# Optimization experiments

Hardware: AMD Instinct MI355X
Metric: run time of the kernel (lower is better)

Reference implementation:

```python
import jax, jax.numpy as jnp
import numpy as np

B, N, C, H, K, R = 128, 512, 7, 64, 16, 2
EPS = 1e-5


def setup_inputs() -> dict:
    key = jax.random.key(0)
    ks = jax.random.split(key, 8)
    def w(k, shape, scale):
        return jax.random.normal(k, shape, jnp.float32) * scale
    return {
        'x':    jax.random.normal(ks[0], (B, C, N), jnp.float32),
        # track_mlp: Conv1d(C->H, bias=False) + BN + ReLU, Conv1d(H->H) + BN + ReLU
        'w_t1': w(ks[1], (H, C), 0.3),
        'g_t1': jnp.ones((H,), jnp.float32), 'b_t1': jnp.zeros((H,), jnp.float32),
        'w_t2': w(ks[2], (H, H), 0.15),
        'g_t2': jnp.ones((H,), jnp.float32), 'b_t2': jnp.zeros((H,), jnp.float32),
        # per-round neighbor MLP: Conv1d(2H->H, bias=False) + BN + ReLU (stacked over rounds)
        'w_nb': w(ks[3], (R, H, 2 * H), 0.1),
        'g_nb': jnp.ones((R, H), jnp.float32), 'b_nb': jnp.zeros((R, H), jnp.float32),
        # scorer: Conv1d(H->H, bias=False) + BN + ReLU, Conv1d(H->1, bias=True)
        'w_s1': w(ks[4], (H, H), 0.15),
        'g_s1': jnp.ones((H,), jnp.float32), 'b_s1': jnp.zeros((H,), jnp.float32),
        'w_s2': w(ks[5], (1, H), 0.15), 'b_s2': jnp.zeros((1,), jnp.float32),
    }


def _conv1x1(w, h):
    # Conv1d with kernel_size=1, no bias: (O,C) x (B,C,N) -> (B,O,N)
    return jnp.einsum('oc,bcn->bon', w, h)


def _bn(h, g, b):
    # eval-mode BatchNorm1d with running_mean=0, running_var=1
    s = g / jnp.sqrt(1.0 + EPS)
    return h * s[None, :, None] + b[None, :, None]


def _knn_idx(h, k):
    # h: (B,H,N); squared euclidean distances in feature space, k nearest (incl. self)
    sq = jnp.sum(h * h, axis=1)                       # (B,N)
    inner = jnp.einsum('bhn,bhm->bnm', h, h)          # (B,N,N)
    d = sq[:, :, None] + sq[:, None, :] - 2.0 * inner  # (B,N,N)
    _, idx = jax.lax.top_k(-d, k)                     # (B,N,K)
    return jax.lax.stop_gradient(idx)


def _edgeconv_round(h, w, g, b, k):
    idx = _knn_idx(h, k)                              # (B,N,K)
    # gather neighbor features: (B,H,1,N) indexed along last axis -> (B,H,N,K)
    nbr = jnp.take_along_axis(h[:, :, None, :], idx[:, None, :, :], axis=3)
    hc = h[:, :, :, None]                             # (B,H,N,1)
    edge = jnp.concatenate([jnp.broadcast_to(hc, nbr.shape), nbr - hc], axis=1)  # (B,2H,N,K)
    bsz, twoh, n, kk = edge.shape
    m = _conv1x1(w, edge.reshape(bsz, twoh, n * kk))  # (B,H,N*K)
    m = jax.nn.relu(_bn(m, g, b)).reshape(bsz, -1, n, kk)
    return jnp.max(m, axis=3)                          # (B,H,N) max aggregation


def reference(x, w_t1, g_t1, b_t1, w_t2, g_t2, b_t2, w_nb, g_nb, b_nb,
              w_s1, g_s1, b_s1, w_s2, b_s2):
    # shared per-track MLP
    h = jax.nn.relu(_bn(_conv1x1(w_t1, x), g_t1, b_t1))
    h = jax.nn.relu(_bn(_conv1x1(w_t2, h), g_t2, b_t2))
    # kNN message-passing rounds (EdgeConv with max aggregation)
    for r in range(w_nb.shape[0]):
        h = _edgeconv_round(h, w_nb[r], g_nb[r], b_nb[r], K)
    # scorer head -> per-track logits (B,1,N)
    h = jax.nn.relu(_bn(_conv1x1(w_s1, h), g_s1, b_s1))
    logits = _conv1x1(w_s2, h) + b_s2[None, :, None]
    return logits
```

## Files before the change

### kernel.cpp

```cpp
#include <hip/hip_runtime.h>
#include <math.h>

#define Bn 128
#define Nn 512
#define Cc 7
#define Hh 64
#define Kk 16
#define Rr 2
#define EPSf 1e-5f

typedef __attribute__((ext_vector_type(8))) short bf16x8;
typedef __attribute__((ext_vector_type(4))) float f32x4;

#define PLN ((size_t)4194304)

__device__ __forceinline__ void split3(float a, short &hs, short &ms, short &ls) {
    unsigned u  = __float_as_uint(a);
    unsigned hu = u & 0xFFFF0000u;
    float r1 = a - __uint_as_float(hu);
    unsigned mu = __float_as_uint(r1) & 0xFFFF0000u;
    float r2 = r1 - __uint_as_float(mu);
    unsigned lu = __float_as_uint(r2) & 0xFFFF0000u;
    hs = (short)(hu >> 16); ms = (short)(mu >> 16); ls = (short)(lu >> 16);
}

#define MFMA6(acc, AH, AM, AL, BH, BM, BL) \
    acc = __builtin_amdgcn_mfma_f32_16x16x32_bf16(AL, BH, acc, 0, 0, 0); \
    acc = __builtin_amdgcn_mfma_f32_16x16x32_bf16(AM, BM, acc, 0, 0, 0); \
    acc = __builtin_amdgcn_mfma_f32_16x16x32_bf16(AH, BL, acc, 0, 0, 0); \
    acc = __builtin_amdgcn_mfma_f32_16x16x32_bf16(AM, BH, acc, 0, 0, 0); \
    acc = __builtin_amdgcn_mfma_f32_16x16x32_bf16(AH, BM, acc, 0, 0, 0); \
    acc = __builtin_amdgcn_mfma_f32_16x16x32_bf16(AH, BH, acc, 0, 0, 0);

__global__ void k_prep(const float* __restrict__ w_nb, const float* __restrict__ w_t2,
                       const float* __restrict__ w_s1, short* __restrict__ wS)
{
    int i = blockIdx.x * 256 + threadIdx.x;
    short h_, m_, l_;
    if (i < 8192) {
        int r = i >> 12, oc = i & 4095;
        int o = oc >> 6, c = oc & 63;
        const float* wr = w_nb + (size_t)r * Hh * 2 * Hh + (size_t)o * 2 * Hh;
        float wc = wr[c], wd = wr[Hh + c];
        short* base = wS + (size_t)r * 6 * 4096;
        split3(wd, h_, m_, l_);
        base[0 * 4096 + oc] = h_; base[1 * 4096 + oc] = m_; base[2 * 4096 + oc] = l_;
        split3(wc - wd, h_, m_, l_);
        base[3 * 4096 + oc] = h_; base[4 * 4096 + oc] = m_; base[5 * 4096 + oc] = l_;
    } else {
        int which = (i - 8192) >> 12;
        int oc = i & 4095;
        const float* src = which ? w_s1 : w_t2;
        short* base = wS + (size_t)(12 + which * 3) * 4096;
        split3(src[oc], h_, m_, l_);
        base[0 * 4096 + oc] = h_; base[1 * 4096 + oc] = m_; base[2 * 4096 + oc] = l_;
    }
}

__global__ __launch_bounds__(256) void k_t12(
    const float* __restrict__ x,
    const float* __restrict__ w1, const float* __restrict__ g1, const float* __restrict__ b1,
    const short* __restrict__ wS2, const float* __restrict__ g2, const float* __restrict__ b2,
    short* __restrict__ hS, float* __restrict__ sq)
{
    __shared__ short wLDS[3][64 * 80];
    __shared__ short h1S[3][16 * 80];
    __shared__ float sqP[16][4];

    int t  = threadIdx.x;
    int p0 = blockIdx.x * 16;
    int b  = p0 >> 9, n0 = p0 & 511;

#pragma unroll
    for (int it = 0; it < 6; ++it) {
        int f = it * 256 + t;
        int plane = f >> 9, i8 = f & 511;
        int o = i8 >> 3, c8 = i8 & 7;
        uint4 v = ((const uint4*)(wS2 + (size_t)plane * 4096))[i8];
        *(uint4*)&wLDS[plane][o * 80 + c8 * 8] = v;
    }

    {
        int pt = t & 15, ow = t >> 4;
        const float inv = rsqrtf(1.0f + EPSf);
        float xv[Cc];
#pragma unroll
        for (int c = 0; c < Cc; ++c)
            xv[c] = x[(b * Cc + c) * Nn + n0 + pt];
#pragma unroll
        for (int j = 0; j < 4; ++j) {
            int o = ow + 16 * j;
            float acc = 0.0f;
#pragma unroll
            for (int c = 0; c < Cc; ++c)
                acc = fmaf(w1[o * Cc + c], xv[c], acc);
            acc = fmaf(acc, g1[o] * inv, b1[o]);
            acc = fmaxf(acc, 0.0f);
            short hs_, ms_, ls_;
            split3(acc, hs_, ms_, ls_);
            h1S[0][pt * 80 + o] = hs_;
            h1S[1][pt * 80 + o] = ms_;
            h1S[2][pt * 80 + o] = ls_;
        }
    }
    __syncthreads();

    int wv = t >> 6, lane = t & 63, col = lane & 15, quad = lane >> 4;
    const float inv = rsqrtf(1.0f + EPSf);

    f32x4 acc = (f32x4){0.f, 0.f, 0.f, 0.f};
#pragma unroll
    for (int ks = 0; ks < 2; ++ks) {
        int aoff = ks * 32 + quad * 8;
        bf16x8 AH = *(bf16x8*)&h1S[0][col * 80 + aoff];
        bf16x8 AM = *(bf16x8*)&h1S[1][col * 80 + aoff];
        bf16x8 AL = *(bf16x8*)&h1S[2][col * 80 + aoff];
        int boff = (wv * 16 + col) * 80 + aoff;
        bf16x8 BH = *(bf16x8*)&wLDS[0][boff];
        bf16x8 BM = *(bf16x8*)&wLDS[1][boff];
        bf16x8 BL = *(bf16x8*)&wLDS[2][boff];
        MFMA6(acc, AH, AM, AL, BH, BM, BL)
    }

    int o = wv * 16 + col;
    float sc = g2[o] * inv, bo = b2[o];
    float s4[4];
#pragma unroll
    for (int r = 0; r < 4; ++r) {
        int pt = quad * 4 + r;
        float a2 = fmaf(acc[r], sc, bo);
        a2 = fmaxf(a2, 0.0f);
        short hs_, ms_, ls_;
        split3(a2, hs_, ms_, ls_);
        size_t rowp = (size_t)(p0 + pt) * Hh + o;
        hS[0 * PLN + rowp] = hs_;
        hS[1 * PLN + rowp] = ms_;
        hS[2 * PLN + rowp] = ls_;
        s4[r] = a2 * a2;
    }
#pragma unroll
    for (int sh = 1; sh < 16; sh <<= 1) {
#pragma unroll
        for (int r = 0; r < 4; ++r) s4[r] += __shfl_xor(s4[r], sh, 64);
    }
    if (col == 0) {
#pragma unroll
        for (int r = 0; r < 4; ++r) sqP[quad * 4 + r][wv] = s4[r];
    }
    __syncthreads();
    if (t < 16) sq[p0 + t] = sqP[t][0] + sqP[t][1] + sqP[t][2] + sqP[t][3];
}

__global__ __launch_bounds__(256, 4) void k_knn(
    const short* __restrict__ hS, const float* __restrict__ sq, int* __restrict__ idxout)
{
    int xcd = blockIdx.x & 7;
    int s_  = blockIdx.x >> 3;
    int b   = xcd + ((s_ >> 5) << 3);
    int n0  = (s_ & 31) << 4;
    int t   = threadIdx.x;

    __shared__ unsigned int keysLDS[16 * 512];
    __shared__ float sqS[512];

    if (t < 128) ((float4*)sqS)[t] = ((const float4*)(sq + (size_t)b * Nn))[t];
    __syncthreads();

    int wv = t >> 6, lane = t & 63, col = lane & 15, quad = lane >> 4;
    const size_t rowbase = (size_t)b * Nn * Hh;

    bf16x8 AH[2], AM[2], AL[2];
    {
        const short* crow = hS + rowbase + (size_t)(n0 + col) * Hh;
#pragma unroll
        for (int ks = 0; ks < 2; ++ks) {
            int aoff = ks * 32 + quad * 8;
            AH[ks] = *(const bf16x8*)(crow + 0 * PLN + aoff);
            AM[ks] = *(const bf16x8*)(crow + 1 * PLN + aoff);
            AL[ks] = *(const bf16x8*)(crow + 2 * PLN + aoff);
        }
    }
    float sqcr[4];
#pragma unroll
    for (int r_ = 0; r_ < 4; ++r_) sqcr[r_] = sqS[n0 + quad * 4 + r_];

    for (int i = 0; i < 8; ++i) {
        int nt = wv * 8 + i;
        const short* prow = hS + rowbase + (size_t)(nt * 16 + col) * Hh;
        f32x4 acc = (f32x4){0.f, 0.f, 0.f, 0.f};
#pragma unroll
        for (int ks = 0; ks < 2; ++ks) {
            int aoff = ks * 32 + quad * 8;
            bf16x8 BH = *(const bf16x8*)(prow + 0 * PLN + aoff);
            bf16x8 BM = *(const bf16x8*)(prow + 1 * PLN + aoff);
            bf16x8 BL = *(const bf16x8*)(prow + 2 * PLN + aoff);
            MFMA6(acc, AH[ks], AM[ks], AL[ks], BH, BM, BL)
        }
        float sqp = sqS[nt * 16 + col];
#pragma unroll
        for (int r_ = 0; r_ < 4; ++r_) {
            int ctr = quad * 4 + r_;
            float d = sqcr[r_] + sqp - 2.0f * acc[r_];
            unsigned int u = __float_as_uint(d);
            u = ((int)u < 0) ? ~u : (u | 0x80000000u);
            keysLDS[ctr * 512 + nt * 16 + col] = u;
        }
    }
    __syncthreads();

    unsigned int kk[4][8];
    int rr[4][8];
#pragma unroll
    for (int s = 0; s < 4; ++s) {
        int jj = wv * 4 + s;
        const uint4* kp = (const uint4*)&keysLDS[jj * 512 + (lane << 3)];
        uint4 A = kp[0], Bq = kp[1];
        kk[s][0] = A.x;  kk[s][1] = A.y;  kk[s][2] = A.z;  kk[s][3] = A.w;
        kk[s][4] = Bq.x; kk[s][5] = Bq.y; kk[s][6] = Bq.z; kk[s][7] = Bq.w;
#pragma unroll
        for (int q = 0; q < 8; ++q) rr[s][q] = q;
    }

#define CE(s, i, j_) { \
    bool sw = (kk[s][i] > kk[s][j_]) || (kk[s][i] == kk[s][j_] && rr[s][i] > rr[s][j_]); \
    unsigned int tk = sw ? kk[s][i] : kk[s][j_]; kk[s][i] = sw ? kk[s][j_] : kk[s][i]; kk[s][j_] = tk; \
    int tr = sw ? rr[s][i] : rr[s][j_]; rr[s][i] = sw ? rr[s][j_] : rr[s][i]; rr[s][j_] = tr; }
#pragma unroll
    for (int s = 0; s < 4; ++s) {
        CE(s,0,1) CE(s,2,3) CE(s,4,5) CE(s,6,7)
        CE(s,0,2) CE(s,1,3) CE(s,4,6) CE(s,5,7)
        CE(s,1,2) CE(s,5,6)
        CE(s,0,4) CE(s,1,5) CE(s,2,6) CE(s,3,7)
        CE(s,2,4) CE(s,3,5)
        CE(s,1,2) CE(s,3,4) CE(s,5,6)
    }
#undef CE

    int outbase[4];
#pragma unroll
    for (int s = 0; s < 4; ++s) outbase[s] = (b * Nn + n0 + wv * 4 + s) * Kk;

    for (int iter = 0; iter < Kk; ++iter) {
        unsigned int mv[4];
#pragma unroll
        for (int s = 0; s < 4; ++s) mv[s] = kk[s][0];
#define DSTEP(ctrl) { \
        _Pragma("unroll") \
        for (int s = 0; s < 4; ++s) { \
            unsigned int ov = (unsigned int)__builtin_amdgcn_update_dpp((int)mv[s], (int)mv[s], ctrl, 0xF, 0xF, false); \
            mv[s] = (ov < mv[s]) ? ov : mv[s]; } }
        DSTEP(0xB1)
        DSTEP(0x4E)
        DSTEP(0x124)
        DSTEP(0x128)
        DSTEP(0x142)
        DSTEP(0x143)
#undef DSTEP
        unsigned int m[4];
#pragma unroll
        for (int s = 0; s < 4; ++s)
            m[s] = (unsigned int)__builtin_amdgcn_readlane((int)mv[s], 63);
#pragma unroll
        for (int s = 0; s < 4; ++s) {
            unsigned long long bal = __ballot(kk[s][0] == m[s]);
            int wn = __ffsll(bal) - 1;
            if (lane == wn) {
                idxout[outbase[s] + iter] = (lane << 3) + rr[s][0];
#pragma unroll
                for (int q = 0; q < 7; ++q) { kk[s][q] = kk[s][q + 1]; rr[s][q] = rr[s][q + 1]; }
                kk[s][7] = 0xFFFFFFFFu;
            }
        }
    }
}

__global__ __launch_bounds__(256, 4) void k_edge(
    const short* __restrict__ hS,
    const int* __restrict__ idx,
    const short* __restrict__ wS,
    const float* __restrict__ g, const float* __restrict__ bb_,
    short* __restrict__ hSout, float* __restrict__ sqout)
{
    __shared__ short wLDS[3][64 * 72];
    __shared__ float baseS[16 * 68];
    __shared__ int   idxS[256];

    int t   = threadIdx.x;
    int xcd = blockIdx.x & 7;
    int s_  = blockIdx.x >> 3;
    int b   = xcd + ((s_ >> 5) << 3);
    int p0  = b * Nn + ((s_ & 31) << 4);

    idxS[t] = idx[p0 * Kk + t];
#pragma unroll
    for (int it = 0; it < 6; ++it) {
        int f = it * 256 + t;
        int plane = f >> 9;
        int i8 = f & 511;
        int o = i8 >> 3, c8 = i8 & 7;
        uint4 v = ((const uint4*)(wS + (size_t)(3 + plane) * 4096))[i8];
        *(uint4*)&wLDS[plane][o * 72 + c8 * 8] = v;
    }
    __syncthreads();

    int wv = t >> 6, lane = t & 63, col = lane & 15, quad = lane >> 4;

    {
        f32x4 bacc = (f32x4){0.f, 0.f, 0.f, 0.f};
        const short* hrow = hS + (size_t)(p0 + col) * Hh;
#pragma unroll
        for (int ks = 0; ks < 2; ++ks) {
            int aoff = ks * 32 + quad * 8;
            bf16x8 AH = *(const bf16x8*)(hrow + 0 * PLN + aoff);
            bf16x8 AM = *(const bf16x8*)(hrow + 1 * PLN + aoff);
            bf16x8 AL = *(const bf16x8*)(hrow + 2 * PLN + aoff);
            int boff = (wv * 16 + col) * 72 + aoff;
            bf16x8 BH = *(bf16x8*)&wLDS[0][boff];
            bf16x8 BM = *(bf16x8*)&wLDS[1][boff];
            bf16x8 BL = *(bf16x8*)&wLDS[2][boff];
            MFMA6(bacc, AH, AM, AL, BH, BM, BL)
        }
#pragma unroll
        for (int r_ = 0; r_ < 4; ++r_)
            baseS[(quad * 4 + r_) * 68 + wv * 16 + col] = bacc[r_];
    }
    __syncthreads();

#pragma unroll
    for (int it = 0; it < 6; ++it) {
        int f = it * 256 + t;
        int plane = f >> 9;
        int i8 = f & 511;
        int o = i8 >> 3, c8 = i8 & 7;
        uint4 v = ((const uint4*)(wS + (size_t)plane * 4096))[i8];
        *(uint4*)&wLDS[plane][o * 72 + c8 * 8] = v;
    }
    __syncthreads();

    const float inv = rsqrtf(1.0f + EPSf);
    float scv[4], bov[4];
#pragma unroll
    for (int nt = 0; nt < 4; ++nt) {
        scv[nt] = g[nt * 16 + col] * inv;
        bov[nt] = bb_[nt * 16 + col];
    }

    for (int pr = 0; pr < 2; ++pr) {
        bf16x8 A[2][2][3];
#pragma unroll
        for (int pt2 = 0; pt2 < 2; ++pt2) {
            int pl = wv * 4 + pr * 2 + pt2;
            int j = idxS[pl * 16 + col];
            const short* nrow = hS + ((size_t)(b * Nn) + j) * Hh;
#pragma unroll
            for (int ks = 0; ks < 2; ++ks) {
                int aoff = ks * 32 + quad * 8;
                A[pt2][ks][0] = *(const bf16x8*)(nrow + 0 * PLN + aoff);
                A[pt2][ks][1] = *(const bf16x8*)(nrow + 1 * PLN + aoff);
                A[pt2][ks][2] = *(const bf16x8*)(nrow + 2 * PLN + aoff);
            }
        }

        f32x4 acc[2][4];
#pragma unroll
        for (int pt2 = 0; pt2 < 2; ++pt2)
#pragma unroll
            for (int nt = 0; nt < 4; ++nt)
                acc[pt2][nt] = (f32x4){0.f, 0.f, 0.f, 0.f};

#pragma unroll
        for (int ks = 0; ks < 2; ++ks)
#pragma unroll
            for (int nt = 0; nt < 4; ++nt) {
                int boff = (nt * 16 + col) * 72 + ks * 32 + quad * 8;
                bf16x8 BH = *(bf16x8*)&wLDS[0][boff];
                bf16x8 BM = *(bf16x8*)&wLDS[1][boff];
                bf16x8 BL = *(bf16x8*)&wLDS[2][boff];
#pragma unroll
                for (int pt2 = 0; pt2 < 2; ++pt2) {
                    f32x4 a = acc[pt2][nt];
                    MFMA6(a, A[pt2][ks][0], A[pt2][ks][1], A[pt2][ks][2], BH, BM, BL)
                    acc[pt2][nt] = a;
                }
            }

#pragma unroll
        for (int pt2 = 0; pt2 < 2; ++pt2) {
            int pl = wv * 4 + pr * 2 + pt2;
            int pglob = p0 + pl;
            float res[4];
#pragma unroll
            for (int nt = 0; nt < 4; ++nt) {
                float base = baseS[pl * 68 + nt * 16 + col];
                f32x4 a = acc[pt2][nt];
                float v0 = fmaf(base + a[0], scv[nt], bov[nt]);
                float v1 = fmaf(base + a[1], scv[nt], bov[nt]);
                float v2 = fmaf(base + a[2], scv[nt], bov[nt]);
                float v3 = fmaf(base + a[3], scv[nt], bov[nt]);
                float vm = fmaxf(fmaxf(v0, v1), fmaxf(v2, v3));
                vm = fmaxf(vm, __shfl_xor(vm, 16));
                vm = fmaxf(vm, __shfl_xor(vm, 32));
                res[nt] = fmaxf(vm, 0.0f);
            }
            float rv = res[quad];
            short hs_, ms_, ls_;
            split3(rv, hs_, ms_, ls_);
            hSout[0 * PLN + (size_t)pglob * Hh + lane] = hs_;
            hSout[1 * PLN + (size_t)pglob * Hh + lane] = ms_;
            hSout[2 * PLN + (size_t)pglob * Hh + lane] = ls_;

            float s = res[0] * res[0] + res[1] * res[1]
                    + res[2] * res[2] + res[3] * res[3];
            s += __shfl_xor(s, 1);
            s += __shfl_xor(s, 2);
            s += __shfl_xor(s, 4);
            s += __shfl_xor(s, 8);
            if (lane == 0) sqout[pglob] = s;
        }
    }
}

__global__ __launch_bounds__(256) void k_head(
    const short* __restrict__ hS, const short* __restrict__ wSs1,
    const float* __restrict__ g1, const float* __restrict__ b1,
    const float* __restrict__ w2, const float* __restrict__ b2,
    float* __restrict__ out)
{
    __shared__ short wLDS[3][64 * 80];
    __shared__ float partS[16][4];

    int t  = threadIdx.x;
    int p0 = blockIdx.x * 16;

#pragma unroll
    for (int it = 0; it < 6; ++it) {
        int f = it * 256 + t;
        int plane = f >> 9, i8 = f & 511;
        int o = i8 >> 3, c8 = i8 & 7;
        uint4 v = ((const uint4*)(wSs1 + (size_t)plane * 4096))[i8];
        *(uint4*)&wLDS[plane][o * 80 + c8 * 8] = v;
    }
    __syncthreads();

    int wv = t >> 6, lane = t & 63, col = lane & 15, quad = lane >> 4;

    const short* crow = hS + (size_t)(p0 + col) * Hh;
    f32x4 acc = (f32x4){0.f, 0.f, 0.f, 0.f};
#pragma unroll
    for (int ks = 0; ks < 2; ++ks) {
        int aoff = ks * 32 + quad * 8;
        bf16x8 AH = *(const bf16x8*)(crow + 0 * PLN + aoff);
        bf16x8 AM = *(const bf16x8*)(crow + 1 * PLN + aoff);
        bf16x8 AL = *(const bf16x8*)(crow + 2 * PLN + aoff);
        int boff = (wv * 16 + col) * 80 + aoff;
        bf16x8 BH = *(bf16x8*)&wLDS[0][boff];
        bf16x8 BM = *(bf16x8*)&wLDS[1][boff];
        bf16x8 BL = *(bf16x8*)&wLDS[2][boff];
        MFMA6(acc, AH, AM, AL, BH, BM, BL)
    }

    int o = wv * 16 + col;
    const float inv = rsqrtf(1.0f + EPSf);
    float sc = g1[o] * inv, bo = b1[o], w2o = w2[o];
    float s4[4];
#pragma unroll
    for (int r = 0; r < 4; ++r) {
        float a = fmaxf(fmaf(acc[r], sc, bo), 0.0f);
        s4[r] = a * w2o;
    }
#pragma unroll
    for (int sh = 1; sh < 16; sh <<= 1) {
#pragma unroll
        for (int r = 0; r < 4; ++r) s4[r] += __shfl_xor(s4[r], sh, 64);
    }
    if (col == 0) {
#pragma unroll
        for (int r = 0; r < 4; ++r) partS[quad * 4 + r][wv] = s4[r];
    }
    __syncthreads();
    if (t < 16)
        out[p0 + t] = partS[t][0] + partS[t][1] + partS[t][2] + partS[t][3] + b2[0];
}

extern "C" void kernel_launch(void* const* d_in, const int* in_sizes, int n_in,
                              void* d_out, int out_size, void* d_ws, size_t ws_size,
                              hipStream_t stream)
{
    const float* x    = (const float*)d_in[0];
    const float* w_t1 = (const float*)d_in[1];
    const float* g_t1 = (const float*)d_in[2];
    const float* b_t1 = (const float*)d_in[3];
    const float* w_t2 = (const float*)d_in[4];
    const float* g_t2 = (const float*)d_in[5];
    const float* b_t2 = (const float*)d_in[6];
    const float* w_nb = (const float*)d_in[7];
    const float* g_nb = (const float*)d_in[8];
    const float* b_nb = (const float*)d_in[9];
    const float* w_s1 = (const float*)d_in[10];
    const float* g_s1 = (const float*)d_in[11];
    const float* b_s1 = (const float*)d_in[12];
    const float* w_s2 = (const float*)d_in[13];
    const float* b_s2 = (const float*)d_in[14];
    float* out = (float*)d_out;

    float* sq  = (float*)d_ws;
    int*   idx = (int*)(sq + (size_t)Bn * Nn);
    short* hSa = (short*)(idx + (size_t)Bn * Nn * Kk);
    short* hSb = hSa + 3 * PLN;
    short* wS  = hSb + 3 * PLN;

    k_prep<<<64, 256, 0, stream>>>(w_nb, w_t2, w_s1, wS);
    k_t12<<<Bn * Nn / 16, 256, 0, stream>>>(x, w_t1, g_t1, b_t1,
                                            wS + (size_t)12 * 4096, g_t2, b_t2,
                                            hSa, sq);

    const short* hSin = hSa;
    short* hSout = hSb;
    for (int r = 0; r < Rr; ++r) {
        k_knn<<<Bn * (Nn / 16), 256, 0, stream>>>(hSin, sq, idx);
        k_edge<<<Bn * Nn / 16, 256, 0, stream>>>(hSin, idx,
            wS + (size_t)r * 6 * 4096, g_nb + r * Hh, b_nb + r * Hh,
            hSout, sq);
        const short* ts = hSout; hSout = (short*)hSin; hSin = ts;
    }
    k_head<<<Bn * Nn / 16, 256, 0, stream>>>(hSin, wS + (size_t)15 * 4096,
                                             g_s1, b_s1, w_s2, b_s2, out);
}
```

Measured before the change: 474.1 us.

## Split kNN kernel into global-memory Gram and top-k selection kernels

The fused kNN kernel, which held a 32 KB LDS key buffer and four rows of sort registers per wave, is split in two. One kernel computes the distance keys and writes them to global memory. A second kernel gives each wave one row to select the top 16 from. This cuts LDS and register pressure so more blocks can be resident. In exchange, the 128x512x512 key matrix (about 128 MB) is written and read back through global memory each round, plus one extra launch.

```diff
diff --git a/kernel.cpp b/kernel.cpp
--- a/kernel.cpp
+++ b/kernel.cpp
@@ -151,8 +151,9 @@
     if (t < 16) sq[p0 + t] = sqP[t][0] + sqP[t][1] + sqP[t][2] + sqP[t][3];
 }
 
-__global__ __launch_bounds__(256, 4) void k_knn(
-    const short* __restrict__ hS, const float* __restrict__ sq, int* __restrict__ idxout)
+__global__ __launch_bounds__(256) void k_gram(
+    const short* __restrict__ hS, const float* __restrict__ sq,
+    unsigned int* __restrict__ keysG)
 {
     int xcd = blockIdx.x & 7;
     int s_  = blockIdx.x >> 3;
@@ -160,9 +161,7 @@
     int n0  = (s_ & 31) << 4;
     int t   = threadIdx.x;
 
-    __shared__ unsigned int keysLDS[16 * 512];
     __shared__ float sqS[512];
-
     if (t < 128) ((float4*)sqS)[t] = ((const float4*)(sq + (size_t)b * Nn))[t];
     __syncthreads();
 
@@ -183,6 +182,8 @@
     float sqcr[4];
 #pragma unroll
     for (int r_ = 0; r_ < 4; ++r_) sqcr[r_] = sqS[n0 + quad * 4 + r_];
+
+    unsigned int* kout = keysG + ((size_t)b * Nn + n0) * Nn;
 
     for (int i = 0; i < 8; ++i) {
         int nt = wv * 8 + i;
@@ -203,52 +204,52 @@
             float d = sqcr[r_] + sqp - 2.0f * acc[r_];
             unsigned int u = __float_as_uint(d);
             u = ((int)u < 0) ? ~u : (u | 0x80000000u);
-            keysLDS[ctr * 512 + nt * 16 + col] = u;
-        }
-    }
-    __syncthreads();
-
-    unsigned int kk[4][8];
-    int rr[4][8];
-#pragma unroll
-    for (int s = 0; s < 4; ++s) {
-        int jj = wv * 4 + s;
-        const uint4* kp = (const uint4*)&keysLDS[jj * 512 + (lane << 3)];
+            kout[(size_t)ctr * Nn + nt * 16 + col] = u;
+        }
+    }
+}
+
+__global__ __launch_bounds__(256) void k_sel(
+    const unsigned int* __restrict__ keysG, int* __restrict__ idxout)
+{
+    int xcd = blockIdx.x & 7;
+    int s_  = blockIdx.x >> 3;
+    int b   = xcd + ((s_ >> 7) << 3);
+    int n0  = (s_ & 127) << 2;
+    int t   = threadIdx.x;
+    int wv  = t >> 6, lane = t & 63;
+    int jj  = n0 + wv;
+
+    unsigned int kk[8];
+    int rr[8];
+    {
+        const uint4* kp = (const uint4*)(keysG + ((size_t)b * Nn + jj) * Nn + (lane << 3));
         uint4 A = kp[0], Bq = kp[1];
-        kk[s][0] = A.x;  kk[s][1] = A.y;  kk[s][2] = A.z;  kk[s][3] = A.w;
-        kk[s][4] = Bq.x; kk[s][5] = Bq.y; kk[s][6] = Bq.z; kk[s][7] = Bq.w;
-#pragma unroll
-        for (int q = 0; q < 8; ++q) rr[s][q] = q;
-    }
-
-#define CE(s, i, j_) { \
-    bool sw = (kk[s][i] > kk[s][j_]) || (kk[s][i] == kk[s][j_] && rr[s][i] > rr[s][j_]); \
-    unsigned int tk = sw ? kk[s][i] : kk[s][j_]; kk[s][i] = sw ? kk[s][j_] : kk[s][i]; kk[s][j_] = tk; \
-    int tr = sw ? rr[s][i] : rr[s][j_]; rr[s][i] = sw ? rr[s][j_] : rr[s][i]; rr[s][j_] = tr; }
-#pragma unroll
-    for (int s = 0; s < 4; ++s) {
-        CE(s,0,1) CE(s,2,3) CE(s,4,5) CE(s,6,7)
-        CE(s,0,2) CE(s,1,3) CE(s,4,6) CE(s,5,7)
-        CE(s,1,2) CE(s,5,6)
-        CE(s,0,4) CE(s,1,5) CE(s,2,6) CE(s,3,7)
-        CE(s,2,4) CE(s,3,5)
-        CE(s,1,2) CE(s,3,4) CE(s,5,6)
-    }
+        kk[0] = A.x;  kk[1] = A.y;  kk[2] = A.z;  kk[3] = A.w;
+        kk[4] = Bq.x; kk[5] = Bq.y; kk[6] = Bq.z; kk[7] = Bq.w;
+#pragma unroll
+        for (int q = 0; q < 8; ++q) rr[q] = q;
+    }
+
+#define CE(i, j_) { \
+    bool sw = (kk[i] > kk[j_]) || (kk[i] == kk[j_] && rr[i] > rr[j_]); \
+    unsigned int tk = sw ? kk[i] : kk[j_]; kk[i] = sw ? kk[j_] : kk[i]; kk[j_] = tk; \
+    int tr = sw ? rr[i] : rr[j_]; rr[i] = sw ? rr[j_] : rr[i]; rr[j_] = tr; }
+    CE(0,1) CE(2,3) CE(4,5) CE(6,7)
+    CE(0,2) CE(1,3) CE(4,6) CE(5,7)
+    CE(1,2) CE(5,6)
+    CE(0,4) CE(1,5) CE(2,6) CE(3,7)
+    CE(2,4) CE(3,5)
+    CE(1,2) CE(3,4) CE(5,6)
 #undef CE
 
-    int outbase[4];
-#pragma unroll
-    for (int s = 0; s < 4; ++s) outbase[s] = (b * Nn + n0 + wv * 4 + s) * Kk;
+    int outbase = (b * Nn + jj) * Kk;
 
     for (int iter = 0; iter < Kk; ++iter) {
-        unsigned int mv[4];
-#pragma unroll
-        for (int s = 0; s < 4; ++s) mv[s] = kk[s][0];
+        unsigned int mv = kk[0];
 #define DSTEP(ctrl) { \
-        _Pragma("unroll") \
-        for (int s = 0; s < 4; ++s) { \
-            unsigned int ov = (unsigned int)__builtin_amdgcn_update_dpp((int)mv[s], (int)mv[s], ctrl, 0xF, 0xF, false); \
-            mv[s] = (ov < mv[s]) ? ov : mv[s]; } }
+        unsigned int ov = (unsigned int)__builtin_amdgcn_update_dpp((int)mv, (int)mv, ctrl, 0xF, 0xF, false); \
+        mv = (ov < mv) ? ov : mv; }
         DSTEP(0xB1)
         DSTEP(0x4E)
         DSTEP(0x124)
@@ -256,20 +257,14 @@
         DSTEP(0x142)
         DSTEP(0x143)
 #undef DSTEP
-        unsigned int m[4];
-#pragma unroll
-        for (int s = 0; s < 4; ++s)
-            m[s] = (unsigned int)__builtin_amdgcn_readlane((int)mv[s], 63);
-#pragma unroll
-        for (int s = 0; s < 4; ++s) {
-            unsigned long long bal = __ballot(kk[s][0] == m[s]);
-            int wn = __ffsll(bal) - 1;
-            if (lane == wn) {
-                idxout[outbase[s] + iter] = (lane << 3) + rr[s][0];
-#pragma unroll
-                for (int q = 0; q < 7; ++q) { kk[s][q] = kk[s][q + 1]; rr[s][q] = rr[s][q + 1]; }
-                kk[s][7] = 0xFFFFFFFFu;
-            }
+        unsigned int m = (unsigned int)__builtin_amdgcn_readlane((int)mv, 63);
+        unsigned long long bal = __ballot(kk[0] == m);
+        int wn = __ffsll(bal) - 1;
+        if (lane == wn) {
+            idxout[outbase + iter] = (lane << 3) + rr[0];
+#pragma unroll
+            for (int q = 0; q < 7; ++q) { kk[q] = kk[q + 1]; rr[q] = rr[q + 1]; }
+            kk[7] = 0xFFFFFFFFu;
         }
     }
 }
@@ -508,6 +503,7 @@
     short* hSa = (short*)(idx + (size_t)Bn * Nn * Kk);
     short* hSb = hSa + 3 * PLN;
     short* wS  = hSb + 3 * PLN;
+    unsigned int* keysG = (unsigned int*)(wS + (size_t)18 * 4096);
 
     k_prep<<<64, 256, 0, stream>>>(w_nb, w_t2, w_s1, wS);
     k_t12<<<Bn * Nn / 16, 256, 0, stream>>>(x, w_t1, g_t1, b_t1,
@@ -517,7 +513,8 @@
     const short* hSin = hSa;
     short* hSout = hSb;
     for (int r = 0; r < Rr; ++r) {
-        k_knn<<<Bn * (Nn / 16), 256, 0, stream>>>(hSin, sq, idx);
+        k_gram<<<Bn * (Nn / 16), 256, 0, stream>>>(hSin, sq, keysG);
+        k_sel<<<Bn * (Nn / 4), 256, 0, stream>>>(keysG, idx);
         k_edge<<<Bn * Nn / 16, 256, 0, stream>>>(hSin, idx,
             wS + (size_t)r * 6 * 4096, g_nb + r * Hh, b_nb + r * Hh,
             hSout, sq);
```

Measured after the change: 545.2 us. 15.0% more time.
